# Kernel optimization log

Hardware: AMD Instinct MI355X
Metric: run time of the kernel (lower is better)

Reference implementation:

```python
import jax, jax.numpy as jnp
import numpy as np

B, N, C_IN, C_H, NUM_CLASSES, E = 2048, 64, 512, 128, 2, 1024


def setup_inputs() -> dict:
    key = jax.random.key(0)
    ks = jax.random.split(key, 6)
    x = jax.random.normal(ks[0], (B, N, C_IN), dtype=jnp.float32)
    edge_index = jax.random.randint(ks[1], (2, E), 0, N, dtype=jnp.int64)
    W1 = jax.random.normal(ks[2], (C_IN, C_H), dtype=jnp.float32) / np.sqrt(C_IN)
    b1 = jnp.zeros((C_H,), jnp.float32)
    W2 = jax.random.normal(ks[3], (C_H, C_H), dtype=jnp.float32) / np.sqrt(C_H)
    b2 = jnp.zeros((C_H,), jnp.float32)
    fcW = jax.random.normal(ks[4], (C_H * N, NUM_CLASSES), dtype=jnp.float32) / np.sqrt(C_H * N)
    fcb = jnp.zeros((NUM_CLASSES,), jnp.float32)
    return {"x": x, "edge_index": edge_index, "W1": W1, "b1": b1,
            "W2": W2, "b2": b2, "fcW": fcW, "fcb": fcb}


def gcn_conv(x, edge_index, W, b):
    # x: [B, N, C]; GCNConv with added self-loops and symmetric normalization:
    # out = D^-1/2 (A + I) D^-1/2 (x W) + b
    n = x.shape[1]
    loops = jnp.arange(n, dtype=edge_index.dtype)
    src = jnp.concatenate([edge_index[0], loops])  # [E+N]
    dst = jnp.concatenate([edge_index[1], loops])  # [E+N]
    deg = jnp.zeros((n,), x.dtype).at[dst].add(1.0)
    norm = jnp.where(deg > 0, jax.lax.rsqrt(jnp.maximum(deg, 1.0)), 0.0)
    h = x @ W  # [B, N, C_out]
    coef = (norm[src] * norm[dst])[None, :, None]  # [1, E+N, 1]
    msg = h[:, src, :] * coef  # gather on shared edge list, batched
    out = jnp.zeros_like(h).at[:, dst, :].add(msg)  # scatter-add aggregation
    return out + b


def reference(x, edge_index, W1, b1, W2, b2, fcW, fcb):
    h = jax.nn.relu(gcn_conv(x, edge_index, W1, b1))
    h = jax.nn.relu(gcn_conv(h, edge_index, W2, b2))
    h = h.reshape(h.shape[0], -1)  # [B, N*C_H]
    return h @ fcW + fcb  # [B, NUM_CLASSES]
```

## Files before the change

kernel.cpp:

```cpp
#include <hip/hip_runtime.h>
#include <cstddef>

#define NN   64
#define CIN  512
#define CH   128

typedef unsigned short ushort_t;
typedef __attribute__((ext_vector_type(8))) short bf16x8;
typedef __attribute__((ext_vector_type(4))) short bf16x4;
typedef __attribute__((ext_vector_type(4))) float f32x4;

__device__ __forceinline__ ushort_t f2bf(float f) {
    union { float f; unsigned u; } v; v.f = f;
    unsigned r = v.u + 0x7fffu + ((v.u >> 16) & 1u);
    return (ushort_t)(r >> 16);
}
__device__ __forceinline__ float bf2f(ushort_t b) {
    union { unsigned u; float f; } v; v.u = ((unsigned)b) << 16;
    return v.f;
}

__global__ __launch_bounds__(256) void prep_all(const int* __restrict__ ei, int E,
                                                const float* __restrict__ W1,
                                                const float* __restrict__ W2,
                                                ushort_t* __restrict__ Ah, ushort_t* __restrict__ Al,
                                                ushort_t* __restrict__ W1h,
                                                ushort_t* __restrict__ W2h) {
    const int t = threadIdx.x;
    if (blockIdx.x == 0) {
        __shared__ float sdeg[NN];
        __shared__ float snorm[NN];
        __shared__ float sA[NN * NN];
        if (t < NN) sdeg[t] = 0.f;
        for (int i = t; i < NN * NN; i += 256) sA[i] = 0.f;
        __syncthreads();
        for (int e = t; e < E; e += 256) atomicAdd(&sdeg[ei[E + e]], 1.0f);
        __syncthreads();
        if (t < NN) snorm[t] = rsqrtf(sdeg[t] + 1.0f);
        __syncthreads();
        for (int e = t; e < E; e += 256) {
            int s = ei[e], d = ei[E + e];
            atomicAdd(&sA[d * NN + s], snorm[s] * snorm[d]);
        }
        if (t < NN) atomicAdd(&sA[t * NN + t], snorm[t] * snorm[t]);
        __syncthreads();
        for (int i = t; i < NN * NN; i += 256) {
            float a = sA[i];
            ushort_t h = f2bf(a);
            Ah[i] = h;
            Al[i] = f2bf(a - bf2f(h));
        }
    } else {
        const int idx = (blockIdx.x - 1) * 256 + t;
        const int stride = 64 * 256;
        for (int i = idx; i < CIN * CH; i += stride) {
            int k = i / CH, c = i % CH;
            W1h[c * CIN + k] = f2bf(W1[i]);
        }
        for (int i = idx; i < CH * CH; i += stride) {
            int k = i / CH, c = i % CH;
            W2h[c * CH + k] = f2bf(W2[i]);
        }
    }
}

__global__ __launch_bounds__(256, 2) void fused_all(
    const float* __restrict__ x,
    const ushort_t* __restrict__ W1h,
    const ushort_t* __restrict__ Ah, const ushort_t* __restrict__ Al,
    const ushort_t* __restrict__ W2h,
    const float* __restrict__ b1, const float* __restrict__ b2,
    const float* __restrict__ fcW, const float* __restrict__ fcb,
    float* __restrict__ out)
{
    __shared__ ushort_t lds[32768];
    __shared__ float sred[16];

    const int t   = threadIdx.x;
    const int l   = t & 63;
    const int w   = t >> 6;
    const int lr  = l & 15;
    const int lk  = l >> 4;
    const int lr7 = lr & 7;
    const size_t rbase = (size_t)blockIdx.x * 128;

    const float* xp0 = x + (rbase + w * 32 + lr) * CIN + lk * 8;
    bf16x8 wreg[4];
    float4 xraw[2][2][2];

    #pragma unroll
    for (int rf = 0; rf < 2; ++rf) {
        const float* xp = xp0 + rf * 16 * CIN;
        xraw[rf][0][0] = *reinterpret_cast<const float4*>(xp);
        xraw[rf][0][1] = *reinterpret_cast<const float4*>(xp + 4);
        xraw[rf][1][0] = *reinterpret_cast<const float4*>(xp + 32);
        xraw[rf][1][1] = *reinterpret_cast<const float4*>(xp + 36);
    }
    #pragma unroll
    for (int u = 0; u < 4; ++u) {
        int q = u * 256 + t, c = q >> 3, g = q & 7;
        wreg[u] = *reinterpret_cast<const bf16x8*>(W1h + (size_t)c * CIN + g * 8);
    }
    #pragma unroll
    for (int u = 0; u < 4; ++u) {
        int q = u * 256 + t, c = q >> 3, g = q & 7;
        *reinterpret_cast<bf16x8*>(&lds[c * 64 + ((g ^ (c & 7)) << 3)]) = wreg[u];
    }
    __syncthreads();

    f32x4 acc[2][8];
    #pragma unroll
    for (int rf = 0; rf < 2; ++rf)
        #pragma unroll
        for (int ct = 0; ct < 8; ++ct)
            #pragma unroll
            for (int i = 0; i < 4; ++i) acc[rf][ct][i] = 0.f;

    for (int kc = 0; kc < 8; ++kc) {
        const ushort_t* sWh = &lds[(kc & 1) * 8192];

        bf16x8 xh[2][2], xl[2][2];
        #pragma unroll
        for (int rf = 0; rf < 2; ++rf)
            #pragma unroll
            for (int ks = 0; ks < 2; ++ks) {
                const float xv[8] = {xraw[rf][ks][0].x, xraw[rf][ks][0].y,
                                     xraw[rf][ks][0].z, xraw[rf][ks][0].w,
                                     xraw[rf][ks][1].x, xraw[rf][ks][1].y,
                                     xraw[rf][ks][1].z, xraw[rf][ks][1].w};
                #pragma unroll
                for (int j = 0; j < 8; ++j) {
                    ushort_t hh = f2bf(xv[j]);
                    xh[rf][ks][j] = (short)hh;
                    xl[rf][ks][j] = (short)f2bf(xv[j] - bf2f(hh));
                }
            }
        if (kc < 7) {
            #pragma unroll
            for (int rf = 0; rf < 2; ++rf) {
                const float* xp = xp0 + rf * 16 * CIN + (kc + 1) * 64;
                xraw[rf][0][0] = *reinterpret_cast<const float4*>(xp);
                xraw[rf][0][1] = *reinterpret_cast<const float4*>(xp + 4);
                xraw[rf][1][0] = *reinterpret_cast<const float4*>(xp + 32);
                xraw[rf][1][1] = *reinterpret_cast<const float4*>(xp + 36);
            }
            #pragma unroll
            for (int u = 0; u < 4; ++u) {
                int q = u * 256 + t, c = q >> 3, g = q & 7;
                wreg[u] = *reinterpret_cast<const bf16x8*>(W1h + (size_t)c * CIN + (kc + 1) * 64 + g * 8);
            }
        }
        #pragma unroll
        for (int ks = 0; ks < 2; ++ks) {
            const int swz = (((ks << 2) | lk) ^ lr7) << 3;
            #pragma unroll
            for (int ct = 0; ct < 8; ++ct) {
                const int c = ct * 16 + lr;
                bf16x8 wh = *reinterpret_cast<const bf16x8*>(&sWh[c * 64 + swz]);
                #pragma unroll
                for (int rf = 0; rf < 2; ++rf) {
                    acc[rf][ct] = __builtin_amdgcn_mfma_f32_16x16x32_bf16(xh[rf][ks], wh, acc[rf][ct], 0, 0, 0);
                    acc[rf][ct] = __builtin_amdgcn_mfma_f32_16x16x32_bf16(xl[rf][ks], wh, acc[rf][ct], 0, 0, 0);
                }
            }
        }
        if (kc < 7) {
            const int nb = ((kc & 1) ^ 1) * 8192;
            #pragma unroll
            for (int u = 0; u < 4; ++u) {
                int q = u * 256 + t, c = q >> 3, g = q & 7;
                *reinterpret_cast<bf16x8*>(&lds[nb + c * 64 + ((g ^ (c & 7)) << 3)]) = wreg[u];
            }
        }
        __syncthreads();
    }


    #pragma unroll
    for (int rf = 0; rf < 2; ++rf) {
        const int grow = w * 32 + rf * 16 + lk * 4;
        const int qb   = grow >> 6;
        const int n0   = grow & 63;
        const int gn   = n0 >> 3, noff = n0 & 7;
        #pragma unroll
        for (int ct = 0; ct < 8; ++ct) {
            const int c = ct * 16 + lr;
            bf16x4 yv;
            #pragma unroll
            for (int r = 0; r < 4; ++r) yv[r] = (short)f2bf(acc[rf][ct][r]);
            *reinterpret_cast<bf16x4*>(&lds[qb * 8192 + c * 64 + ((gn ^ lr7) << 3) + noff]) = yv;
        }
    }
    __syncthreads();

    const int q = w >> 1;
    const int h = w & 1;
    ushort_t* sYtq = &lds[q * 8192];
    ushort_t* sH1q = &lds[16384 + q * 8192];

    bf16x8 ahf[2][2], alf[2][2];
    #pragma unroll
    for (int rf = 0; rf < 2; ++rf)
        #pragma unroll
        for (int ks = 0; ks < 2; ++ks) {
            const int nrow = h * 32 + rf * 16 + lr;
            const int ko = ks * 32 + lk * 8;
            ahf[rf][ks] = *reinterpret_cast<const bf16x8*>(Ah + nrow * NN + ko);
            alf[rf][ks] = *reinterpret_cast<const bf16x8*>(Al + nrow * NN + ko);
        }
    {
        f32x4 hacc[2][8];
        #pragma unroll
        for (int rf = 0; rf < 2; ++rf)
            #pragma unroll
            for (int ct = 0; ct < 8; ++ct)
                #pragma unroll
                for (int i = 0; i < 4; ++i) hacc[rf][ct][i] = 0.f;
        #pragma unroll
        for (int ks = 0; ks < 2; ++ks) {
            const int swz = (((ks << 2) | lk) ^ lr7) << 3;
            #pragma unroll
            for (int ct = 0; ct < 8; ++ct) {
                const int c = ct * 16 + lr;
                bf16x8 y = *reinterpret_cast<const bf16x8*>(&sYtq[c * 64 + swz]);
                #pragma unroll
                for (int rf = 0; rf < 2; ++rf) {
                    hacc[rf][ct] = __builtin_amdgcn_mfma_f32_16x16x32_bf16(ahf[rf][ks], y, hacc[rf][ct], 0, 0, 0);
                    hacc[rf][ct] = __builtin_amdgcn_mfma_f32_16x16x32_bf16(alf[rf][ks], y, hacc[rf][ct], 0, 0, 0);
                }
            }
        }
        #pragma unroll
        for (int rf = 0; rf < 2; ++rf)
            #pragma unroll
            for (int ct = 0; ct < 8; ++ct) {
                const int c = ct * 16 + lr;
                const int gc = c >> 3;
                const float bias = b1[c];
                #pragma unroll
                for (int r = 0; r < 4; ++r) {
                    const int n = h * 32 + rf * 16 + lk * 4 + r;
                    float v = fmaxf(hacc[rf][ct][r] + bias, 0.f);
                    sH1q[n * 128 + ((gc ^ (n & 7)) << 3) + (c & 7)] = f2bf(v);
                }
            }
    }
    __syncthreads();

    #pragma unroll
    for (int u = 0; u < 8; ++u) {
        int idx = u * 256 + t;
        int c = idx >> 4, g = idx & 15;
        *reinterpret_cast<bf16x8*>(&lds[c * 128 + ((g ^ (c & 7)) << 3)]) =
            *reinterpret_cast<const bf16x8*>(W2h + (size_t)c * CH + g * 8);
    }
    __syncthreads();

    f32x4 acc2[2][8];
    #pragma unroll
    for (int rf = 0; rf < 2; ++rf)
        #pragma unroll
        for (int ct = 0; ct < 8; ++ct)
            #pragma unroll
            for (int i = 0; i < 4; ++i) acc2[rf][ct][i] = 0.f;
    {
        bf16x8 hf[2][4];
        #pragma unroll
        for (int rf = 0; rf < 2; ++rf) {
            const int n = h * 32 + rf * 16 + lr;
            #pragma unroll
            for (int ks = 0; ks < 4; ++ks) {
                const int gh = ((ks << 2) | lk) ^ (n & 7);
                hf[rf][ks] = *reinterpret_cast<const bf16x8*>(&sH1q[n * 128 + (gh << 3)]);
            }
        }
        #pragma unroll
        for (int ct = 0; ct < 8; ++ct) {
            const int c = ct * 16 + lr;
            #pragma unroll
            for (int ks = 0; ks < 4; ++ks) {
                const int gw = ((ks << 2) | lk) ^ (c & 7);
                bf16x8 w2 = *reinterpret_cast<const bf16x8*>(&lds[c * 128 + (gw << 3)]);
                #pragma unroll
                for (int rf = 0; rf < 2; ++rf)
                    acc2[rf][ct] = __builtin_amdgcn_mfma_f32_16x16x32_bf16(hf[rf][ks], w2, acc2[rf][ct], 0, 0, 0);
            }
        }
    }
    __syncthreads();

    #pragma unroll
    for (int rf = 0; rf < 2; ++rf) {
        const int n0 = h * 32 + rf * 16 + lk * 4;
        const int gn = n0 >> 3, noff = n0 & 7;
        #pragma unroll
        for (int ct = 0; ct < 8; ++ct) {
            const int c = ct * 16 + lr;
            bf16x4 yv;
            #pragma unroll
            for (int r = 0; r < 4; ++r) yv[r] = (short)f2bf(acc2[rf][ct][r]);
            *reinterpret_cast<bf16x4*>(&sYtq[c * 64 + ((gn ^ lr7) << 3) + noff]) = yv;
        }
    }
    __syncthreads();

    float p0 = 0.f, p1 = 0.f;
    {
        f32x4 h2[2][8];
        #pragma unroll
        for (int rf = 0; rf < 2; ++rf)
            #pragma unroll
            for (int ct = 0; ct < 8; ++ct)
                #pragma unroll
                for (int i = 0; i < 4; ++i) h2[rf][ct][i] = 0.f;
        #pragma unroll
        for (int ks = 0; ks < 2; ++ks) {
            const int swz = (((ks << 2) | lk) ^ lr7) << 3;
            #pragma unroll
            for (int ct = 0; ct < 8; ++ct) {
                const int c = ct * 16 + lr;
                bf16x8 y = *reinterpret_cast<const bf16x8*>(&sYtq[c * 64 + swz]);
                #pragma unroll
                for (int rf = 0; rf < 2; ++rf) {
                    h2[rf][ct] = __builtin_amdgcn_mfma_f32_16x16x32_bf16(ahf[rf][ks], y, h2[rf][ct], 0, 0, 0);
                    h2[rf][ct] = __builtin_amdgcn_mfma_f32_16x16x32_bf16(alf[rf][ks], y, h2[rf][ct], 0, 0, 0);
                }
            }
        }
        #pragma unroll
        for (int rf = 0; rf < 2; ++rf)
            #pragma unroll
            for (int ct = 0; ct < 8; ++ct) {
                const int c = ct * 16 + lr;
                const float bias = b2[c];
                #pragma unroll
                for (int r = 0; r < 4; ++r) {
                    const int n = h * 32 + rf * 16 + lk * 4 + r;
                    float v = fmaxf(h2[rf][ct][r] + bias, 0.f);
                    const float2 fw = *reinterpret_cast<const float2*>(fcW + ((size_t)(n * CH + c)) * 2);
                    p0 = fmaf(v, fw.x, p0);
                    p1 = fmaf(v, fw.y, p1);
                }
            }
    }
    #pragma unroll
    for (int off = 32; off > 0; off >>= 1) {
        p0 += __shfl_down(p0, off);
        p1 += __shfl_down(p1, off);
    }
    if (l == 0) { sred[w * 2] = p0; sred[w * 2 + 1] = p1; }
    __syncthreads();
    if (t == 0) {
        const size_t bA = (size_t)blockIdx.x * 2;
        out[bA * 2 + 0]       = sred[0] + sred[2] + fcb[0];
        out[bA * 2 + 1]       = sred[1] + sred[3] + fcb[1];
        out[(bA + 1) * 2 + 0] = sred[4] + sred[6] + fcb[0];
        out[(bA + 1) * 2 + 1] = sred[5] + sred[7] + fcb[1];
    }
}

extern "C" void kernel_launch(void* const* d_in, const int* in_sizes, int n_in,
                              void* d_out, int out_size, void* d_ws, size_t ws_size,
                              hipStream_t stream) {
    const float* x   = (const float*)d_in[0];
    const int*   ei  = (const int*)d_in[1];
    const float* W1  = (const float*)d_in[2];
    const float* b1  = (const float*)d_in[3];
    const float* W2  = (const float*)d_in[4];
    const float* b2  = (const float*)d_in[5];
    const float* fcW = (const float*)d_in[6];
    const float* fcb = (const float*)d_in[7];
    float* outp = (float*)d_out;

    ushort_t* Ah  = (ushort_t*)d_ws;
    ushort_t* Al  = Ah + NN * NN;
    ushort_t* W1h = Al + NN * NN;
    ushort_t* W2h = W1h + CIN * CH;

    const int E  = in_sizes[1] / 2;
    const int Bn = in_sizes[0] / (NN * CIN);

    prep_all<<<65, 256, 0, stream>>>(ei, E, W1, W2, Ah, Al, W1h, W2h);
    fused_all<<<Bn / 2, 256, 0, stream>>>(x, W1h, Ah, Al, W2h,
                                          b1, b2, fcW, fcb, outp);
}
```

Before: 77.00 us.

## Double block to 512 threads with full W1 resident in LDS

Each block now processes four graphs with 512 threads and loads the whole bf16 W1 (512x128) into a 128 KB LDS buffer once, in place of streaming it in double-buffered 64-wide K chunks. This removes the per-chunk W1 global loads and the per-chunk barriers from the first GEMM loop and halves redundant W1 traffic per graph. In exchange, LDS use grows to about 128 KB per block, which likely allows only one block per CU. The upfront W1 load is also no longer overlapped with compute.

```diff
diff --git a/kernel.cpp b/kernel.cpp
--- a/kernel.cpp
+++ b/kernel.cpp
@@ -64,7 +64,7 @@
     }
 }
 
-__global__ __launch_bounds__(256, 2) void fused_all(
+__global__ __launch_bounds__(512, 2) void fused_all(
     const float* __restrict__ x,
     const ushort_t* __restrict__ W1h,
     const ushort_t* __restrict__ Ah, const ushort_t* __restrict__ Al,
@@ -73,7 +73,7 @@
     const float* __restrict__ fcW, const float* __restrict__ fcb,
     float* __restrict__ out)
 {
-    __shared__ ushort_t lds[32768];
+    __shared__ ushort_t lds[65536];
     __shared__ float sred[16];
 
     const int t   = threadIdx.x;
@@ -82,10 +82,9 @@
     const int lr  = l & 15;
     const int lk  = l >> 4;
     const int lr7 = lr & 7;
-    const size_t rbase = (size_t)blockIdx.x * 128;
+    const size_t rbase = (size_t)blockIdx.x * 256;
 
     const float* xp0 = x + (rbase + w * 32 + lr) * CIN + lk * 8;
-    bf16x8 wreg[4];
     float4 xraw[2][2][2];
 
     #pragma unroll
@@ -97,14 +96,11 @@
         xraw[rf][1][1] = *reinterpret_cast<const float4*>(xp + 36);
     }
     #pragma unroll
-    for (int u = 0; u < 4; ++u) {
-        int q = u * 256 + t, c = q >> 3, g = q & 7;
-        wreg[u] = *reinterpret_cast<const bf16x8*>(W1h + (size_t)c * CIN + g * 8);
-    }
-    #pragma unroll
-    for (int u = 0; u < 4; ++u) {
-        int q = u * 256 + t, c = q >> 3, g = q & 7;
-        *reinterpret_cast<bf16x8*>(&lds[c * 64 + ((g ^ (c & 7)) << 3)]) = wreg[u];
+    for (int u = 0; u < 16; ++u) {
+        int idx = u * 512 + t;
+        int c = idx >> 6, g = idx & 63;
+        *reinterpret_cast<bf16x8*>(&lds[c * 512 + ((g ^ (c & 7)) << 3)]) =
+            *reinterpret_cast<const bf16x8*>(W1h + (size_t)c * CIN + g * 8);
     }
     __syncthreads();
 
@@ -117,8 +113,6 @@
             for (int i = 0; i < 4; ++i) acc[rf][ct][i] = 0.f;
 
     for (int kc = 0; kc < 8; ++kc) {
-        const ushort_t* sWh = &lds[(kc & 1) * 8192];
-
         bf16x8 xh[2][2], xl[2][2];
         #pragma unroll
         for (int rf = 0; rf < 2; ++rf)
@@ -144,19 +138,14 @@
                 xraw[rf][1][0] = *reinterpret_cast<const float4*>(xp + 32);
                 xraw[rf][1][1] = *reinterpret_cast<const float4*>(xp + 36);
             }
-            #pragma unroll
-            for (int u = 0; u < 4; ++u) {
-                int q = u * 256 + t, c = q >> 3, g = q & 7;
-                wreg[u] = *reinterpret_cast<const bf16x8*>(W1h + (size_t)c * CIN + (kc + 1) * 64 + g * 8);
-            }
         }
         #pragma unroll
         for (int ks = 0; ks < 2; ++ks) {
-            const int swz = (((ks << 2) | lk) ^ lr7) << 3;
-            #pragma unroll
-            for (int ct = 0; ct < 8; ++ct) {
-                const int c = ct * 16 + lr;
-                bf16x8 wh = *reinterpret_cast<const bf16x8*>(&sWh[c * 64 + swz]);
+            #pragma unroll
+            for (int ct = 0; ct < 8; ++ct) {
+                const int c = ct * 16 + lr;
+                const int gk = kc * 8 + (((ks << 2) | lk) ^ (c & 7));
+                bf16x8 wh = *reinterpret_cast<const bf16x8*>(&lds[c * 512 + gk * 8]);
                 #pragma unroll
                 for (int rf = 0; rf < 2; ++rf) {
                     acc[rf][ct] = __builtin_amdgcn_mfma_f32_16x16x32_bf16(xh[rf][ks], wh, acc[rf][ct], 0, 0, 0);
@@ -164,16 +153,8 @@
                 }
             }
         }
-        if (kc < 7) {
-            const int nb = ((kc & 1) ^ 1) * 8192;
-            #pragma unroll
-            for (int u = 0; u < 4; ++u) {
-                int q = u * 256 + t, c = q >> 3, g = q & 7;
-                *reinterpret_cast<bf16x8*>(&lds[nb + c * 64 + ((g ^ (c & 7)) << 3)]) = wreg[u];
-            }
-        }
-        __syncthreads();
-    }
+    }
+    __syncthreads();
 
 
     #pragma unroll
@@ -196,7 +177,7 @@
     const int q = w >> 1;
     const int h = w & 1;
     ushort_t* sYtq = &lds[q * 8192];
-    ushort_t* sH1q = &lds[16384 + q * 8192];
+    ushort_t* sH1q = &lds[32768 + q * 8192];
 
     bf16x8 ahf[2][2], alf[2][2];
     #pragma unroll
@@ -248,8 +229,8 @@
     __syncthreads();
 
     #pragma unroll
-    for (int u = 0; u < 8; ++u) {
-        int idx = u * 256 + t;
+    for (int u = 0; u < 4; ++u) {
+        int idx = u * 512 + t;
         int c = idx >> 4, g = idx & 15;
         *reinterpret_cast<bf16x8*>(&lds[c * 128 + ((g ^ (c & 7)) << 3)]) =
             *reinterpret_cast<const bf16x8*>(W2h + (size_t)c * CH + g * 8);
@@ -351,11 +332,12 @@
     if (l == 0) { sred[w * 2] = p0; sred[w * 2 + 1] = p1; }
     __syncthreads();
     if (t == 0) {
-        const size_t bA = (size_t)blockIdx.x * 2;
-        out[bA * 2 + 0]       = sred[0] + sred[2] + fcb[0];
-        out[bA * 2 + 1]       = sred[1] + sred[3] + fcb[1];
-        out[(bA + 1) * 2 + 0] = sred[4] + sred[6] + fcb[0];
-        out[(bA + 1) * 2 + 1] = sred[5] + sred[7] + fcb[1];
+        const size_t bA = (size_t)blockIdx.x * 4;
+        #pragma unroll
+        for (int qb = 0; qb < 4; ++qb) {
+            out[(bA + qb) * 2 + 0] = sred[4 * qb + 0] + sred[4 * qb + 2] + fcb[0];
+            out[(bA + qb) * 2 + 1] = sred[4 * qb + 1] + sred[4 * qb + 3] + fcb[1];
+        }
     }
 }
 
@@ -381,6 +363,6 @@
     const int Bn = in_sizes[0] / (NN * CIN);
 
     prep_all<<<65, 256, 0, stream>>>(ei, E, W1, W2, Ah, Al, W1h, W2h);
-    fused_all<<<Bn / 2, 256, 0, stream>>>(x, W1h, Ah, Al, W2h,
+    fused_all<<<Bn / 4, 512, 0, stream>>>(x, W1h, Ah, Al, W2h,
                                           b1, b2, fcW, fcb, outp);
 }
```

Measured after the change: 83.97 us. 9.0% more time.
